# Optimization experiments

Hardware: AMD Instinct MI355X
Metric: run time of the kernel (lower is better)

Reference implementation:

```python
import jax, jax.numpy as jnp
import numpy as np

N_NODES = 20000
N_EDGES = 320000
L = 128
NODE_IN = 30
EDGE_IN = 4
NUM_LAYERS = 5


def _mlp(x, w1, b1, a, w2, b2):
    # Linear -> PReLU(scalar slope) -> Linear
    h = x @ w1 + b1
    h = jnp.where(h > 0, h, a * h)
    return h @ w2 + b2


def setup_inputs() -> dict:
    key = jax.random.key(0)
    ks = iter(jax.random.split(key, 64))
    s = 0.02

    def w(shape):
        return (s * jax.random.normal(next(ks), shape)).astype(jnp.float32)

    inp = {}
    inp["x"] = jax.random.normal(next(ks), (N_NODES, NODE_IN), dtype=jnp.float32)
    inp["edge_attr"] = jax.random.normal(next(ks), (N_EDGES, EDGE_IN), dtype=jnp.float32)
    inp["edge_index"] = jax.random.randint(next(ks), (2, N_EDGES), 0, N_NODES, dtype=jnp.int32)
    # node encoder
    inp["ne_w1"] = w((NODE_IN, L)); inp["ne_b1"] = jnp.zeros((L,), jnp.float32)
    inp["ne_a"] = jnp.float32(0.25)
    inp["ne_w2"] = w((L, L)); inp["ne_b2"] = jnp.zeros((L,), jnp.float32)
    # edge encoder
    inp["ee_w1"] = w((EDGE_IN, L)); inp["ee_b1"] = jnp.zeros((L,), jnp.float32)
    inp["ee_a"] = jnp.float32(0.25)
    inp["ee_w2"] = w((L, L)); inp["ee_b2"] = jnp.zeros((L,), jnp.float32)
    # processor layers (stacked over NUM_LAYERS)
    inp["le_w1"] = w((NUM_LAYERS, 3 * L, L)); inp["le_b1"] = jnp.zeros((NUM_LAYERS, L), jnp.float32)
    inp["le_a"] = jnp.full((NUM_LAYERS,), 0.25, jnp.float32)
    inp["le_w2"] = w((NUM_LAYERS, L, L)); inp["le_b2"] = jnp.zeros((NUM_LAYERS, L), jnp.float32)
    inp["ln_w1"] = w((NUM_LAYERS, 2 * L, L)); inp["ln_b1"] = jnp.zeros((NUM_LAYERS, L), jnp.float32)
    inp["ln_a"] = jnp.full((NUM_LAYERS,), 0.25, jnp.float32)
    inp["ln_w2"] = w((NUM_LAYERS, L, L)); inp["ln_b2"] = jnp.zeros((NUM_LAYERS, L), jnp.float32)
    # decoder
    inp["de_w1"] = w((L, L)); inp["de_b1"] = jnp.zeros((L,), jnp.float32)
    inp["de_a"] = jnp.float32(0.25)
    inp["de_w2"] = w((L, 3)); inp["de_b2"] = jnp.zeros((3,), jnp.float32)
    return inp


def reference(x, edge_attr, edge_index,
              ne_w1, ne_b1, ne_a, ne_w2, ne_b2,
              ee_w1, ee_b1, ee_a, ee_w2, ee_b2,
              le_w1, le_b1, le_a, le_w2, le_b2,
              ln_w1, ln_b1, ln_a, ln_w2, ln_b2,
              de_w1, de_b1, de_a, de_w2, de_b2):
    n = x.shape[0]
    src = edge_index[0]  # x_j (source)
    dst = edge_index[1]  # x_i (target), aggregation index

    h = _mlp(x, ne_w1, ne_b1, ne_a, ne_w2, ne_b2)            # [N, L]
    e = _mlp(edge_attr, ee_w1, ee_b1, ee_a, ee_w2, ee_b2)    # [E, L]

    for l in range(le_w1.shape[0]):
        m = jnp.concatenate([h[dst], h[src], e], axis=-1)    # [E, 3L]
        m = _mlp(m, le_w1[l], le_b1[l], le_a[l], le_w2[l], le_b2[l])  # [E, L]
        agg = jax.ops.segment_sum(m, dst, num_segments=n)    # [N, L]
        upd = _mlp(jnp.concatenate([h, agg], axis=-1),
                   ln_w1[l], ln_b1[l], ln_a[l], ln_w2[l], ln_b2[l])
        h = h + upd

    return _mlp(h, de_w1, de_b1, de_a, de_w2, de_b2)         # [N, 3]
```

## Files before the change

kernel.cpp:

```cpp
#include <hip/hip_runtime.h>
#include <cstdint>
#include <cstddef>


#define DEVI static __device__ __forceinline__

typedef __bf16 bf16_t;
typedef bf16_t bf16x8 __attribute__((ext_vector_type(8)));
typedef bf16_t bf16x4 __attribute__((ext_vector_type(4)));
typedef float f32x4v __attribute__((ext_vector_type(4)));

DEVI float4 ld4(const float* p) { return *(const float4*)p; }
DEVI void st4(float* p, float4 v) { *(float4*)p = v; }
DEVI float prelu1(float z, float a) { return z > 0.f ? z : a * z; }
DEVI void atomicAddF(float* p, float v) {
  __hip_atomic_fetch_add(p, v, __ATOMIC_RELAXED, __HIP_MEMORY_SCOPE_AGENT);
}
DEVI f32x4v mfma_bf16(bf16x8 a, bf16x8 b, f32x4v c) {
  return __builtin_amdgcn_mfma_f32_16x16x32_bf16(a, b, c, 0, 0, 0);
}
DEVI void mfma3(f32x4v& acc, bf16x8 ah, bf16x8 al, bf16x8 bh, bf16x8 bl) {
  acc = mfma_bf16(ah, bh, acc);
  acc = mfma_bf16(al, bh, acc);
  acc = mfma_bf16(ah, bl, acc);
}
DEVI void split2(float x, bf16_t& h, bf16_t& l) {
  h = (bf16_t)x;
  l = (bf16_t)(x - (float)h);
}
DEVI bf16x8 ldb8(const bf16_t* p) { return *(const bf16x8*)p; }

#define NST 136
#define EST 72


DEVI void stage_f32_c4(const float* __restrict__ src, int row0, int M,
                       int lane, int h, int cH, bf16_t* SAh, bf16_t* SAl)
{
  const int row = h * 16 + (lane >> 2);
  const int grow = row0 + row;
  const int colbase = cH * 64 + (lane & 3) * 16;
  #pragma unroll
  for (int j = 0; j < 4; ++j) {
    int kc = colbase + j * 4;
    float4 v = make_float4(0.f, 0.f, 0.f, 0.f);
    if (grow < M) v = ld4(src + (size_t)grow * 128 + kc);
    bf16_t h0,l0,h1,l1,h2,l2,h3,l3;
    split2(v.x,h0,l0); split2(v.y,h1,l1); split2(v.z,h2,l2); split2(v.w,h3,l3);
    *(bf16x4*)(SAh + row * NST + kc) = (bf16x4){h0,h1,h2,h3};
    *(bf16x4*)(SAl + row * NST + kc) = (bf16x4){l0,l1,l2,l3};
  }
}

DEVI void stage_planes_c4(const bf16_t* __restrict__ gh, const bf16_t* __restrict__ gl,
                          int row0, int M, int lane, int h, int cH,
                          bf16_t* SAh, bf16_t* SAl)
{
  const int row = h * 16 + (lane >> 2);
  const int grow = row0 + row;
  const int colbase = cH * 64 + (lane & 3) * 16;
  #pragma unroll
  for (int j = 0; j < 2; ++j) {
    int kc = colbase + j * 8;
    bf16x8 vh = {};
    bf16x8 vl = {};
    if (grow < M) {
      vh = ldb8(gh + (size_t)grow * 128 + kc);
      vl = ldb8(gl + (size_t)grow * 128 + kc);
    }
    *(bf16x8*)(SAh + row * NST + kc) = vh;
    *(bf16x8*)(SAl + row * NST + kc) = vl;
  }
}

DEVI void gemm_c4(const bf16_t* SAh, const bf16_t* SAl,
                  const bf16_t* __restrict__ BT, f32x4v acc[4],
                  int h, int ntb, int p, int q)
{
  #pragma unroll
  for (int ks = 0; ks < 4; ++ks) {
    const int k0 = ks * 32 + q * 8;
    bf16x8 aH = ldb8(SAh + (h * 16 + p) * NST + k0);
    bf16x8 aL = ldb8(SAl + (h * 16 + p) * NST + k0);
    #pragma unroll
    for (int nt = 0; nt < 4; ++nt) {
      const bf16_t* bp = BT + (size_t)((ntb + nt) * 16 + p) * 128 + k0;
      mfma3(acc[nt], aH, aL, ldb8(bp), ldb8(bp + 16384));
    }
  }
}

DEVI void store_c4(float* __restrict__ O, int row0, int M,
                   const f32x4v acc[4], int h, int cH, int p, int q)
{
  int rb = row0 + h * 16 + q * 4;
  #pragma unroll
  for (int r = 0; r < 4; ++r) {
    if (rb + r < M) {
      float* op = O + (size_t)(rb + r) * 128 + p * 8 + cH * 4;
      st4(op, make_float4(acc[0][r], acc[1][r], acc[2][r], acc[3][r]));
    }
  }
}

DEVI void stage_cregs_c4(const f32x4v acc[4], int h, int cH, int p, int q,
                         bf16_t* SAh, bf16_t* SAl)
{
  #pragma unroll
  for (int r = 0; r < 4; ++r) {
    int row = h * 16 + q * 4 + r;
    bf16x4 vh, vl;
    #pragma unroll
    for (int nt = 0; nt < 4; ++nt) {
      bf16_t hb, lb;
      split2(acc[nt][r], hb, lb);
      vh[nt] = hb; vl[nt] = lb;
    }
    *(bf16x4*)(SAh + row * NST + p * 8 + cH * 4) = vh;
    *(bf16x4*)(SAl + row * NST + p * 8 + cH * 4) = vl;
  }
}

DEVI void planes_out_c4(bf16_t* __restrict__ gh, bf16_t* __restrict__ gl,
                        int row0, int M, int lane, int h, int cH,
                        const bf16_t* SAh, const bf16_t* SAl)
{
  const int row = h * 16 + (lane >> 2);
  const int grow = row0 + row;
  const int colbase = cH * 64 + (lane & 3) * 16;
  if (grow < M) {
    #pragma unroll
    for (int j = 0; j < 2; ++j) {
      int kc = colbase + j * 8;
      *(bf16x8*)(gh + (size_t)grow * 128 + kc) = *(const bf16x8*)(SAh + row * NST + kc);
      *(bf16x8*)(gl + (size_t)grow * 128 + kc) = *(const bf16x8*)(SAl + row * NST + kc);
    }
  }
}

DEVI void ld8f(float dst[8], const float* __restrict__ src, int p) {
  *(float4*)(dst)     = ld4(src + p * 8);
  *(float4*)(dst + 4) = ld4(src + p * 8 + 4);
}

DEVI void ld4f(float dst[4], const float* __restrict__ src, int p, int cH) {
  *(float4*)(dst) = ld4(src + p * 8 + cH * 4);
}

__global__ __launch_bounds__(256, 3) void k_svu(
    float* Sbuf,
    bf16_t* __restrict__ hSh, bf16_t* __restrict__ hSl,
    const bf16_t* __restrict__ WtilT, const bf16_t* __restrict__ Wn1aT,
    const bf16_t* __restrict__ lnw2T, const bf16_t* __restrict__ W1nextT,
    const float* __restrict__ ln_b1_l, const float* __restrict__ btil_l,
    const int* __restrict__ deg, const float* __restrict__ ln_a_l,
    const float* __restrict__ ln_b2_l,
    float* __restrict__ P, float* __restrict__ Q, int doPQ, int M)
{
  __shared__ __align__(16) bf16_t SAh[32 * NST];
  __shared__ __align__(16) bf16_t SAl[32 * NST];
  const int t = threadIdx.x, lane = t & 63, wave = t >> 6;
  const int h = wave & 1, cH = wave >> 1;
  const int p = lane & 15, q = lane >> 4;
  const int row0 = blockIdx.x * 32;

  f32x4v acc1[4];
  #pragma unroll
  for (int j = 0; j < 4; ++j) acc1[j] = (f32x4v){0.f, 0.f, 0.f, 0.f};

  stage_f32_c4(Sbuf, row0, M, lane, h, cH, SAh, SAl);
  {
    const int row = h * 16 + (lane >> 2);
    const int grow = row0 + row;
    const int colbase = cH * 64 + (lane & 3) * 16;
    if (grow < M) {
      float4 z4 = make_float4(0.f, 0.f, 0.f, 0.f);
      #pragma unroll
      for (int j = 0; j < 4; ++j)
        st4(Sbuf + (size_t)grow * 128 + colbase + j * 4, z4);
    }
  }
  __syncthreads();
  gemm_c4(SAh, SAl, WtilT, acc1, h, cH * 4, p, q);
  __syncthreads();
  stage_planes_c4(hSh, hSl, row0, M, lane, h, cH, SAh, SAl);
  __syncthreads();
  gemm_c4(SAh, SAl, Wn1aT, acc1, h, cH * 4, p, q);

  float hold[4][4];
  #pragma unroll
  for (int r = 0; r < 4; ++r) {
    int row = h * 16 + q * 4 + r;
    bf16x4 vh = *(const bf16x4*)(SAh + row * NST + p * 8 + cH * 4);
    bf16x4 vl = *(const bf16x4*)(SAl + row * NST + p * 8 + cH * 4);
    #pragma unroll
    for (int nt = 0; nt < 4; ++nt)
      hold[nt][r] = (float)vh[nt] + (float)vl[nt];
  }
  __syncthreads();

  const float alpha = *ln_a_l;
  float degf[4];
  #pragma unroll
  for (int r = 0; r < 4; ++r) {
    int row = row0 + h * 16 + q * 4 + r;
    degf[r] = (row < M) ? (float)deg[row] : 0.f;
  }
  float b1c[4], btc[4];
  ld4f(b1c, ln_b1_l, p, cH);
  ld4f(btc, btil_l, p, cH);
  #pragma unroll
  for (int nt = 0; nt < 4; ++nt)
    #pragma unroll
    for (int r = 0; r < 4; ++r)
      acc1[nt][r] = prelu1(acc1[nt][r] + b1c[nt] + degf[r] * btc[nt], alpha);

  stage_cregs_c4(acc1, h, cH, p, q, SAh, SAl);
  __syncthreads();
  f32x4v acc2[4];
  #pragma unroll
  for (int j = 0; j < 4; ++j) acc2[j] = (f32x4v){0.f, 0.f, 0.f, 0.f};
  gemm_c4(SAh, SAl, lnw2T, acc2, h, cH * 4, p, q);
  __syncthreads();

  float b2c[4];
  ld4f(b2c, ln_b2_l, p, cH);
  #pragma unroll
  for (int nt = 0; nt < 4; ++nt)
    #pragma unroll
    for (int r = 0; r < 4; ++r)
      acc2[nt][r] = hold[nt][r] + acc2[nt][r] + b2c[nt];

  stage_cregs_c4(acc2, h, cH, p, q, SAh, SAl);
  __syncthreads();
  planes_out_c4(hSh, hSl, row0, M, lane, h, cH, SAh, SAl);

  if (doPQ) {
    f32x4v acc3[4];
    #pragma unroll
    for (int j = 0; j < 4; ++j) acc3[j] = (f32x4v){0.f, 0.f, 0.f, 0.f};
    gemm_c4(SAh, SAl, W1nextT, acc3, h, cH * 4, p, q);
    store_c4(P, row0, M, acc3, h, cH, p, q);
    #pragma unroll
    for (int j = 0; j < 4; ++j) acc3[j] = (f32x4v){0.f, 0.f, 0.f, 0.f};
    gemm_c4(SAh, SAl, W1nextT + 32768, acc3, h, cH * 4, p, q);
    store_c4(Q, row0, M, acc3, h, cH, p, q);
  }
}

__global__ __launch_bounds__(256, 3) void k_enc(
    const float* __restrict__ UN, const bf16_t* __restrict__ new2T,
    const float* __restrict__ b2, const bf16_t* __restrict__ W1T0,
    bf16_t* __restrict__ hSh, bf16_t* __restrict__ hSl,
    float* __restrict__ P, float* __restrict__ Q, int M)
{
  __shared__ __align__(16) bf16_t SAh[32 * NST];
  __shared__ __align__(16) bf16_t SAl[32 * NST];
  const int t = threadIdx.x, lane = t & 63, wave = t >> 6;
  const int h = wave & 1, cH = wave >> 1;
  const int p = lane & 15, q = lane >> 4;
  const int row0 = blockIdx.x * 32;

  f32x4v acc[4];
  #pragma unroll
  for (int j = 0; j < 4; ++j) acc[j] = (f32x4v){0.f, 0.f, 0.f, 0.f};
  stage_f32_c4(UN, row0, M, lane, h, cH, SAh, SAl);
  __syncthreads();
  gemm_c4(SAh, SAl, new2T, acc, h, cH * 4, p, q);
  __syncthreads();
  float b2c[4];
  ld4f(b2c, b2, p, cH);
  #pragma unroll
  for (int nt = 0; nt < 4; ++nt)
    #pragma unroll
    for (int r = 0; r < 4; ++r) acc[nt][r] += b2c[nt];
  stage_cregs_c4(acc, h, cH, p, q, SAh, SAl);
  __syncthreads();
  planes_out_c4(hSh, hSl, row0, M, lane, h, cH, SAh, SAl);

  f32x4v acc3[4];
  #pragma unroll
  for (int j = 0; j < 4; ++j) acc3[j] = (f32x4v){0.f, 0.f, 0.f, 0.f};
  gemm_c4(SAh, SAl, W1T0, acc3, h, cH * 4, p, q);
  store_c4(P, row0, M, acc3, h, cH, p, q);
  #pragma unroll
  for (int j = 0; j < 4; ++j) acc3[j] = (f32x4v){0.f, 0.f, 0.f, 0.f};
  gemm_c4(SAh, SAl, W1T0 + 32768, acc3, h, cH * 4, p, q);
  store_c4(Q, row0, M, acc3, h, cH, p, q);
}

__global__ __launch_bounds__(256, 3) void k_edge(
    const float* __restrict__ sEa, const int* __restrict__ sSrc,
    const int* __restrict__ sDst,
    const int* __restrict__ rowStart, const int* __restrict__ deg,
    const float* __restrict__ ee_w1, const float* __restrict__ ee_b1,
    const float* __restrict__ ee_a,
    const bf16_t* __restrict__ WhatT, const float* __restrict__ bvec,
    const float* __restrict__ alpha_ptr,
    const float* __restrict__ P, const float* __restrict__ Q,
    float* __restrict__ S, int N, int E)
{
  __shared__ __align__(16) float Stile[32 * 132];
  __shared__ __align__(16) float ew[640];
  __shared__ __align__(16) bf16_t Ast[128 * EST];

  const int t = threadIdx.x, lane = t & 63, wave = t >> 6;
  const int p = lane & 15, q = lane >> 4;
  const int e0 = blockIdx.x * 128;
  const int dstLo = sDst[e0];

  for (int i = t; i < 640; i += 256)
    ew[i] = (i < 512) ? ee_w1[i] : ee_b1[i - 512];
  for (int i = t; i < 32 * 132; i += 256) Stile[i] = 0.f;
  __syncthreads();

  const float ua = *ee_a;
  const float alpha = *alpha_ptr;
  float bvc[8];
  ld8f(bvc, bvec, p);

  const int srow = wave * 32 + (lane >> 1);
  const int scb = (lane & 1) * 32;
  float4 eav = make_float4(0.f, 0.f, 0.f, 0.f);
  {
    int ed = e0 + srow;
    if (ed < E) eav = ld4(sEa + (size_t)ed * 4);
  }

  f32x4v acc[2][8];
  #pragma unroll
  for (int i = 0; i < 2; ++i)
    #pragma unroll
    for (int j = 0; j < 8; ++j) acc[i][j] = (f32x4v){0.f, 0.f, 0.f, 0.f};

  for (int c = 0; c < 2; ++c) {
    #pragma unroll
    for (int j = 0; j < 8; ++j) {
      int kc = scb + j * 4;
      int kg = c * 64 + kc;
      float4 w0 = ld4(ew + kg);
      float4 w1 = ld4(ew + 128 + kg);
      float4 w2 = ld4(ew + 256 + kg);
      float4 w3 = ld4(ew + 384 + kg);
      float4 bb = ld4(ew + 512 + kg);
      float ux = bb.x, uy = bb.y, uz = bb.z, uw = bb.w;
      ux = fmaf(eav.x, w0.x, ux); uy = fmaf(eav.x, w0.y, uy);
      uz = fmaf(eav.x, w0.z, uz); uw = fmaf(eav.x, w0.w, uw);
      ux = fmaf(eav.y, w1.x, ux); uy = fmaf(eav.y, w1.y, uy);
      uz = fmaf(eav.y, w1.z, uz); uw = fmaf(eav.y, w1.w, uw);
      ux = fmaf(eav.z, w2.x, ux); uy = fmaf(eav.z, w2.y, uy);
      uz = fmaf(eav.z, w2.z, uz); uw = fmaf(eav.z, w2.w, uw);
      ux = fmaf(eav.w, w3.x, ux); uy = fmaf(eav.w, w3.y, uy);
      uz = fmaf(eav.w, w3.z, uz); uw = fmaf(eav.w, w3.w, uw);
      *(bf16x4*)(Ast + srow * EST + kc) = (bf16x4){
          (bf16_t)prelu1(ux, ua), (bf16_t)prelu1(uy, ua),
          (bf16_t)prelu1(uz, ua), (bf16_t)prelu1(uw, ua)};
    }
    #pragma unroll
    for (int ks = 0; ks < 2; ++ks) {
      const int k0 = ks * 32 + q * 8;
      const int kg = c * 64 + k0;
      bf16x8 aH0 = ldb8(Ast + (wave * 32 + p) * EST + k0);
      bf16x8 aH1 = ldb8(Ast + (wave * 32 + 16 + p) * EST + k0);
      #pragma unroll
      for (int nt = 0; nt < 8; ++nt) {
        const bf16_t* bp = WhatT + (size_t)(nt * 16 + p) * 128 + kg;
        bf16x8 bH = ldb8(bp);
        bf16x8 bL = ldb8(bp + 16384);
        acc[0][nt] = mfma_bf16(aH0, bH, acc[0][nt]);
        acc[0][nt] = mfma_bf16(aH0, bL, acc[0][nt]);
        acc[1][nt] = mfma_bf16(aH1, bH, acc[1][nt]);
        acc[1][nt] = mfma_bf16(aH1, bL, acc[1][nt]);
      }
    }
  }

  #pragma unroll
  for (int mt = 0; mt < 2; ++mt) {
    float rs[8];
    #pragma unroll
    for (int nt = 0; nt < 8; ++nt) rs[nt] = 0.f;
    int curd = -1;
    float pv[8];
    #pragma unroll
    for (int nt = 0; nt < 8; ++nt) pv[nt] = 0.f;
    #pragma unroll
    for (int r = 0; r < 4; ++r) {
      int ed = e0 + wave * 32 + mt * 16 + q * 4 + r;
      if (ed < E) {
        int d = sDst[ed];
        int s = sSrc[ed];
        if (d != curd) {
          if (curd >= 0) {
            int rr = curd - dstLo;
            if (rr < 32) {
              #pragma unroll
              for (int nt = 0; nt < 8; ++nt)
                atomicAdd(&Stile[rr * 132 + p * 8 + nt], rs[nt]);
            } else {
              #pragma unroll
              for (int nt = 0; nt < 8; ++nt)
                atomicAddF(S + (size_t)curd * 128 + p * 8 + nt, rs[nt]);
            }
            #pragma unroll
            for (int nt = 0; nt < 8; ++nt) rs[nt] = 0.f;
          }
          curd = d;
          ld8f(pv, P + (size_t)d * 128, p);
          #pragma unroll
          for (int nt = 0; nt < 8; ++nt) pv[nt] += bvc[nt];
        }
        float qv[8];
        ld8f(qv, Q + (size_t)s * 128, p);
        #pragma unroll
        for (int nt = 0; nt < 8; ++nt) {
          float z = acc[mt][nt][r] + pv[nt] + qv[nt];
          rs[nt] += prelu1(z, alpha);
        }
      }
    }
    if (curd >= 0) {
      int rr = curd - dstLo;
      if (rr < 32) {
        #pragma unroll
        for (int nt = 0; nt < 8; ++nt)
          atomicAdd(&Stile[rr * 132 + p * 8 + nt], rs[nt]);
      } else {
        #pragma unroll
        for (int nt = 0; nt < 8; ++nt)
          atomicAddF(S + (size_t)curd * 128 + p * 8 + nt, rs[nt]);
      }
    }
  }
  __syncthreads();

  const int lastE = (e0 + 127 < E) ? (e0 + 127) : (E - 1);
  const int dstHi = sDst[lastE];
  const int col4 = (t & 31) * 4;
  #pragma unroll
  for (int rr0 = 0; rr0 < 32; rr0 += 8) {
    int rr = rr0 + (t >> 5);
    int d = dstLo + rr;
    if (d <= dstHi && d < N) {
      float4 v = ld4(&Stile[rr * 132 + col4]);
      bool interior = (rowStart[d] >= e0) && (rowStart[d] + deg[d] <= e0 + 128);
      float* sp = S + (size_t)d * 128 + col4;
      if (interior) {
        st4(sp, v);
      } else {
        atomicAddF(sp + 0, v.x); atomicAddF(sp + 1, v.y);
        atomicAddF(sp + 2, v.z); atomicAddF(sp + 3, v.w);
      }
    }
  }
}

__global__ __launch_bounds__(128, 4) void k_dec(
    const bf16_t* __restrict__ hSh, const bf16_t* __restrict__ hSl,
    const bf16_t* __restrict__ dw1T,
    const float* __restrict__ de_b1, const float* __restrict__ de_a,
    const float* __restrict__ de_w2, const float* __restrict__ de_b2,
    float* __restrict__ out, int M)
{
  __shared__ __align__(16) float Cs[32][132];
  __shared__ __align__(16) float w2s[384];
  const int t = threadIdx.x, lane = t & 63, wave = t >> 6;
  const int p = lane & 15, q = lane >> 4;
  const int row0 = blockIdx.x * 32;
  for (int i = t; i < 384; i += 128) w2s[i] = de_w2[i];

  f32x4v acc[8];
  #pragma unroll
  for (int j = 0; j < 8; ++j) acc[j] = (f32x4v){0.f, 0.f, 0.f, 0.f};
  const size_t ra = (size_t)(row0 + wave * 16 + p) * 128;
  #pragma unroll
  for (int ks = 0; ks < 4; ++ks) {
    const int k0 = ks * 32 + q * 8;
    bf16x8 aH = ldb8(hSh + ra + k0);
    bf16x8 aL = ldb8(hSl + ra + k0);
    #pragma unroll
    for (int nt = 0; nt < 8; ++nt) {
      const bf16_t* bp = dw1T + (size_t)(nt * 16 + p) * 128 + k0;
      mfma3(acc[nt], aH, aL, ldb8(bp), ldb8(bp + 16384));
    }
  }
  const float alpha = *de_a;
  float b1c[8];
  ld8f(b1c, de_b1, p);
  #pragma unroll
  for (int r = 0; r < 4; ++r) {
    int row = wave * 16 + q * 4 + r;
    float* cp = &Cs[row][p * 8];
    st4(cp, make_float4(prelu1(acc[0][r] + b1c[0], alpha),
                        prelu1(acc[1][r] + b1c[1], alpha),
                        prelu1(acc[2][r] + b1c[2], alpha),
                        prelu1(acc[3][r] + b1c[3], alpha)));
    st4(cp + 4, make_float4(prelu1(acc[4][r] + b1c[4], alpha),
                            prelu1(acc[5][r] + b1c[5], alpha),
                            prelu1(acc[6][r] + b1c[6], alpha),
                            prelu1(acc[7][r] + b1c[7], alpha)));
  }
  __syncthreads();
  if (t < 32) {
    float s0 = de_b2[0], s1 = de_b2[1], s2 = de_b2[2];
    for (int k = 0; k < 128; ++k) {
      float vv = Cs[t][k];
      s0 = fmaf(vv, w2s[k * 3 + 0], s0);
      s1 = fmaf(vv, w2s[k * 3 + 1], s1);
      s2 = fmaf(vv, w2s[k * 3 + 2], s2);
    }
    int row = row0 + t;
    if (row < M) {
      out[(size_t)row * 3 + 0] = s0;
      out[(size_t)row * 3 + 1] = s1;
      out[(size_t)row * 3 + 2] = s2;
    }
  }
}

__global__ __launch_bounds__(256) void k_tsplit(
    const float* __restrict__ ne_w2, const float* __restrict__ de_w1,
    const float* __restrict__ le_w1, const float* __restrict__ ln_w1,
    const float* __restrict__ ln_w2, bf16_t* __restrict__ WT)
{
  int jid = blockIdx.x;
  const float* src; int slot;
  if (jid == 0)      { src = ne_w2; slot = 0; }
  else if (jid == 1) { src = de_w1; slot = 1; }
  else {
    int l = (jid - 2) >> 2, wj = (jid - 2) & 3;
    slot = 2 + l * 6 + wj;
    src = (wj == 0) ? le_w1 + (size_t)l * 49152
        : (wj == 1) ? le_w1 + (size_t)l * 49152 + 16384
        : (wj == 2) ? ln_w1 + (size_t)l * 32768
                    : ln_w2 + (size_t)l * 16384;
  }
  bf16_t* oh = WT + (size_t)slot * 32768;
  bf16_t* ol = oh + 16384;
  const int base = blockIdx.y * 2048;
  for (int idx = base + threadIdx.x; idx < base + 2048; idx += 256) {
    int k = idx >> 7, n = idx & 127;
    bf16_t hb, lb;
    split2(src[idx], hb, lb);
    int pos = ((n & 7) * 16 + (n >> 3)) * 128 + k;
    oh[pos] = hb;
    ol[pos] = lb;
  }
}

__global__ __launch_bounds__(256) void k_fold(
    const float* __restrict__ ee_w2, const float* __restrict__ ee_b2,
    const float* __restrict__ le_w1, const float* __restrict__ le_b1,
    const float* __restrict__ le_w2, const float* __restrict__ le_b2,
    const float* __restrict__ ln_w1,
    bf16_t* __restrict__ WT, float* __restrict__ bvec, float* __restrict__ btil)
{
  const int l = blockIdx.x;
  const int which = blockIdx.y;
  const int z = blockIdx.z;
  const float* L; const float* Rm; const float* lb; const float* badd;
  int slot; float* bout;
  if (which == 0) {
    L = ee_w2; Rm = le_w1 + (size_t)l * 49152 + 256 * 128;
    lb = ee_b2; badd = le_b1 + l * 128;
    slot = 2 + l * 6 + 4; bout = bvec + l * 128;
  } else {
    L = le_w2 + (size_t)l * 16384; Rm = ln_w1 + (size_t)l * 32768 + 128 * 128;
    lb = le_b2 + l * 128; badd = nullptr;
    slot = 2 + l * 6 + 5; bout = btil + l * 128;
  }
  bf16_t* oh = WT + (size_t)slot * 32768;
  bf16_t* ol = oh + 16384;
  const int t = threadIdx.x;
  const int base = z * 512;
  for (int eidx = base + t; eidx < base + 512; eidx += 256) {
    int k = eidx >> 7, n = eidx & 127;
    float a = 0.f;
    for (int d = 0; d < 128; d += 4) {
      float4 lv = ld4(L + k * 128 + d);
      a = fmaf(lv.x, Rm[(d + 0) * 128 + n], a);
      a = fmaf(lv.y, Rm[(d + 1) * 128 + n], a);
      a = fmaf(lv.z, Rm[(d + 2) * 128 + n], a);
      a = fmaf(lv.w, Rm[(d + 3) * 128 + n], a);
    }
    bf16_t hb, lbv;
    split2(a, hb, lbv);
    int pos = ((n & 7) * 16 + (n >> 3)) * 128 + k;
    oh[pos] = hb;
    ol[pos] = lbv;
  }
  if (z == 0 && t < 128) {
    float a = badd ? badd[t] : 0.f;
    for (int d = 0; d < 128; ++d) a = fmaf(lb[d], Rm[d * 128 + t], a);
    bout[t] = a;
  }
}

__global__ __launch_bounds__(256) void k_node_u(
    const float* __restrict__ x, const float* __restrict__ w1,
    const float* __restrict__ b1, const float* __restrict__ a_ptr,
    float* __restrict__ U, int M)
{
  int gid = blockIdx.x * 256 + threadIdx.x;
  int m = gid >> 5;
  if (m >= M) return;
  int nc = (gid & 31) << 2;
  float a = *a_ptr;
  float4 bb = ld4(b1 + nc);
  float z0 = bb.x, z1 = bb.y, z2 = bb.z, z3 = bb.w;
  const float* xr = x + (size_t)m * 30;
  #pragma unroll
  for (int j = 0; j < 30; ++j) {
    float xv = xr[j];
    float4 wv = ld4(w1 + j * 128 + nc);
    z0 = fmaf(xv, wv.x, z0); z1 = fmaf(xv, wv.y, z1);
    z2 = fmaf(xv, wv.z, z2); z3 = fmaf(xv, wv.w, z3);
  }
  st4(U + (size_t)m * 128 + nc,
      make_float4(prelu1(z0, a), prelu1(z1, a), prelu1(z2, a), prelu1(z3, a)));
}

__global__ void k_hist(const int* __restrict__ dstIdx, int* __restrict__ deg, int E) {
  int i = blockIdx.x * 256 + threadIdx.x;
  if (i < E) atomicAdd(deg + dstIdx[i], 1);
}

__global__ __launch_bounds__(1024) void k_scan(
    const int* __restrict__ deg, int* __restrict__ cursor,
    int* __restrict__ rowStart, int N, int per)
{
  __shared__ int part[1024];
  const int t = threadIdx.x;
  const int base = t * per;
  int local = 0;
  for (int i = 0; i < per; ++i) {
    int idx = base + i;
    if (idx < N) local += deg[idx];
  }
  part[t] = local;
  __syncthreads();
  for (int off = 1; off < 1024; off <<= 1) {
    int v = (t >= off) ? part[t - off] : 0;
    __syncthreads();
    part[t] += v;
    __syncthreads();
  }
  int run = (t == 0) ? 0 : part[t - 1];
  for (int i = 0; i < per; ++i) {
    int idx = base + i;
    if (idx < N) {
      cursor[idx] = run;
      rowStart[idx] = run;
      run += deg[idx];
    }
  }
}

__global__ void k_scatter(const int* __restrict__ srcIdx, const int* __restrict__ dstIdx,
                          const float* __restrict__ ea, int* __restrict__ cursor,
                          int* __restrict__ sSrc, int* __restrict__ sDst,
                          float* __restrict__ sEa, int E)
{
  int e = blockIdx.x * 256 + threadIdx.x;
  if (e < E) {
    int d = dstIdx[e];
    int p = atomicAdd(cursor + d, 1);
    sSrc[p] = srcIdx[e];
    sDst[p] = d;
    st4(sEa + (size_t)p * 4, ld4(ea + (size_t)e * 4));
  }
}

extern "C" void kernel_launch(void* const* d_in, const int* in_sizes, int n_in,
                              void* d_out, int out_size, void* d_ws, size_t ws_size,
                              hipStream_t stream)
{
  const float* x     = (const float*)d_in[0];
  const float* ea    = (const float*)d_in[1];
  const int*   ei    = (const int*)  d_in[2];
  const float* ne_w1 = (const float*)d_in[3];
  const float* ne_b1 = (const float*)d_in[4];
  const float* ne_a  = (const float*)d_in[5];
  const float* ne_w2 = (const float*)d_in[6];
  const float* ne_b2 = (const float*)d_in[7];
  const float* ee_w1 = (const float*)d_in[8];
  const float* ee_b1 = (const float*)d_in[9];
  const float* ee_a  = (const float*)d_in[10];
  const float* ee_w2 = (const float*)d_in[11];
  const float* ee_b2 = (const float*)d_in[12];
  const float* le_w1 = (const float*)d_in[13];
  const float* le_b1 = (const float*)d_in[14];
  const float* le_a  = (const float*)d_in[15];
  const float* le_w2 = (const float*)d_in[16];
  const float* le_b2 = (const float*)d_in[17];
  const float* ln_w1 = (const float*)d_in[18];
  const float* ln_b1 = (const float*)d_in[19];
  const float* ln_a  = (const float*)d_in[20];
  const float* ln_w2 = (const float*)d_in[21];
  const float* ln_b2 = (const float*)d_in[22];
  const float* de_w1 = (const float*)d_in[23];
  const float* de_b1 = (const float*)d_in[24];
  const float* de_a  = (const float*)d_in[25];
  const float* de_w2 = (const float*)d_in[26];
  const float* de_b2 = (const float*)d_in[27];

  const int N = in_sizes[0] / 30;
  const int E = in_sizes[1] / 4;
  const int* srcIdx = ei;
  const int* dstIdx = ei + E;

  const int g32 = (N + 31) / 32;
  const int gE  = (E + 127) / 128;
  const int Np = g32 * 32;
  const size_t NNp = (size_t)Np * 128;

  float* w = (float*)d_ws;
  float* Pb   = w; w += NNp;
  float* Qb   = w; w += NNp;
  float* Sb   = w; w += NNp;
  float* bvec = w; w += 5 * 128;
  float* btil = w; w += 5 * 128;
  float* sEa  = w; w += (size_t)E * 4;
  bf16_t* hSh = (bf16_t*)w;
  bf16_t* hSl = hSh + NNp;  w += NNp;
  bf16_t* WT  = (bf16_t*)w; w += 32 * 32768 / 2;
  int* ip     = (int*)w;
  int* deg    = ip; ip += N;
  int* cursor = ip; ip += N;
  int* rowStart = ip; ip += N;
  int* sSrc   = ip; ip += E;
  int* sDst   = ip; ip += E;

  float* out = (float*)d_out;

  k_tsplit<<<dim3(22, 8), dim3(256), 0, stream>>>(ne_w2, de_w1, le_w1, ln_w1, ln_w2, WT);
  k_fold<<<dim3(5, 2, 32), dim3(256), 0, stream>>>(ee_w2, ee_b2, le_w1, le_b1,
                                                   le_w2, le_b2, ln_w1, WT, bvec, btil);
  hipMemsetAsync(deg, 0, (size_t)N * 4, stream);
  k_hist<<<dim3((E + 255) / 256), dim3(256), 0, stream>>>(dstIdx, deg, E);
  k_scan<<<dim3(1), dim3(1024), 0, stream>>>(deg, cursor, rowStart, N,
                                             (N + 1023) / 1024);
  k_scatter<<<dim3((E + 255) / 256), dim3(256), 0, stream>>>(
      srcIdx, dstIdx, ea, cursor, sSrc, sDst, sEa, E);

  k_node_u<<<dim3((N * 32 + 255) / 256), dim3(256), 0, stream>>>(x, ne_w1, ne_b1, ne_a, Sb, N);
  k_enc<<<dim3(g32), dim3(256), 0, stream>>>(Sb, WT, ne_b2, WT + 2 * 32768,
                                             hSh, hSl, Pb, Qb, N);

  hipMemsetAsync(Sb, 0, (size_t)N * 128 * 4, stream);

  for (int l = 0; l < 5; ++l) {
    const bf16_t* slotL = WT + (size_t)(2 + l * 6) * 32768;
    k_edge<<<dim3(gE), dim3(256), 0, stream>>>(
        sEa, sSrc, sDst, rowStart, deg, ee_w1, ee_b1, ee_a,
        slotL + 4 * 32768, bvec + l * 128, le_a + l, Pb, Qb, Sb, N, E);
    const bf16_t* W1next = (l < 4) ? (WT + (size_t)(2 + (l + 1) * 6) * 32768) : WT;
    k_svu<<<dim3(g32), dim3(256), 0, stream>>>(
        Sb, hSh, hSl, slotL + 5 * 32768, slotL + 2 * 32768, slotL + 3 * 32768,
        W1next, ln_b1 + (size_t)l * 128, btil + l * 128, deg, ln_a + l,
        ln_b2 + (size_t)l * 128, Pb, Qb, (l < 4) ? 1 : 0, N);
  }

  k_dec<<<dim3(g32), dim3(128), 0, stream>>>(hSh, hSl, WT + 32768, de_b1, de_a,
                                             de_w2, de_b2, out, N);
}
```

Before: 1.334 ms.

## Fuse node encoder first layer into k_enc and decoder into last k_svu

Computes the node encoder's first linear+PReLU inside k_enc from shared-memory copies of x and ne_w1, so the separate k_node_u kernel and its fp32 intermediate round trip go away. The final update layer now also runs the decoder MLP in place, skipping the hSh/hSl write and the separate k_dec launch. k_edge's launch-bounds occupancy hint is raised from 3 to 4 blocks. The extra shared memory in k_enc and the larger k_svu could lower occupancy, and the raised k_edge hint may cause register spilling.

```diff
diff --git a/kernel.cpp b/kernel.cpp
--- a/kernel.cpp
+++ b/kernel.cpp
@@ -155,10 +155,18 @@
     const float* __restrict__ ln_b1_l, const float* __restrict__ btil_l,
     const int* __restrict__ deg, const float* __restrict__ ln_a_l,
     const float* __restrict__ ln_b2_l,
-    float* __restrict__ P, float* __restrict__ Q, int doPQ, int M)
-{
-  __shared__ __align__(16) bf16_t SAh[32 * NST];
-  __shared__ __align__(16) bf16_t SAl[32 * NST];
+    float* __restrict__ P, float* __restrict__ Q, int doPQ,
+    const bf16_t* __restrict__ dw1T, const float* __restrict__ de_b1,
+    const float* __restrict__ de_a, const float* __restrict__ de_w2,
+    const float* __restrict__ de_b2, float* __restrict__ outp,
+    int doDec, int M)
+{
+  __shared__ __align__(16) char SMEM[2 * 32 * NST * 2];
+  __shared__ __align__(16) float w2s[384];
+  bf16_t* SAh = (bf16_t*)SMEM;
+  bf16_t* SAl = (bf16_t*)(SMEM + 32 * NST * 2);
+  float*  Cs  = (float*)SMEM;
+
   const int t = threadIdx.x, lane = t & 63, wave = t >> 6;
   const int h = wave & 1, cH = wave >> 1;
   const int p = lane & 15, q = lane >> 4;
@@ -232,6 +240,50 @@
       acc2[nt][r] = hold[nt][r] + acc2[nt][r] + b2c[nt];
 
   stage_cregs_c4(acc2, h, cH, p, q, SAh, SAl);
+
+  if (doDec) {
+    if (t < 128) {
+      w2s[t] = de_w2[t]; w2s[t + 128] = de_w2[t + 128]; w2s[t + 256] = de_w2[t + 256];
+    }
+    __syncthreads();
+    f32x4v acc3[4];
+    #pragma unroll
+    for (int j = 0; j < 4; ++j) acc3[j] = (f32x4v){0.f, 0.f, 0.f, 0.f};
+    gemm_c4(SAh, SAl, dw1T, acc3, h, cH * 4, p, q);
+    const float da = *de_a;
+    float db1[4];
+    ld4f(db1, de_b1, p, cH);
+    #pragma unroll
+    for (int nt = 0; nt < 4; ++nt)
+      #pragma unroll
+      for (int r = 0; r < 4; ++r)
+        acc3[nt][r] = prelu1(acc3[nt][r] + db1[nt], da);
+    __syncthreads();
+    #pragma unroll
+    for (int r = 0; r < 4; ++r) {
+      int row = h * 16 + q * 4 + r;
+      st4(&Cs[row * 132 + p * 8 + cH * 4],
+          make_float4(acc3[0][r], acc3[1][r], acc3[2][r], acc3[3][r]));
+    }
+    __syncthreads();
+    if (t < 32) {
+      float s0 = de_b2[0], s1 = de_b2[1], s2 = de_b2[2];
+      for (int k = 0; k < 128; ++k) {
+        float vv = Cs[t * 132 + k];
+        s0 = fmaf(vv, w2s[k * 3 + 0], s0);
+        s1 = fmaf(vv, w2s[k * 3 + 1], s1);
+        s2 = fmaf(vv, w2s[k * 3 + 2], s2);
+      }
+      int row = row0 + t;
+      if (row < M) {
+        outp[(size_t)row * 3 + 0] = s0;
+        outp[(size_t)row * 3 + 1] = s1;
+        outp[(size_t)row * 3 + 2] = s2;
+      }
+    }
+    return;
+  }
+
   __syncthreads();
   planes_out_c4(hSh, hSl, row0, M, lane, h, cH, SAh, SAl);
 
@@ -249,23 +301,65 @@
 }
 
 __global__ __launch_bounds__(256, 3) void k_enc(
-    const float* __restrict__ UN, const bf16_t* __restrict__ new2T,
+    const float* __restrict__ x, const float* __restrict__ ne_w1,
+    const float* __restrict__ ne_b1, const float* __restrict__ ne_a,
+    const bf16_t* __restrict__ new2T,
     const float* __restrict__ b2, const bf16_t* __restrict__ W1T0,
     bf16_t* __restrict__ hSh, bf16_t* __restrict__ hSl,
     float* __restrict__ P, float* __restrict__ Q, int M)
 {
   __shared__ __align__(16) bf16_t SAh[32 * NST];
   __shared__ __align__(16) bf16_t SAl[32 * NST];
+  __shared__ __align__(16) float w1s[30 * 128];
+  __shared__ __align__(16) float xs[32 * 30];
+  __shared__ __align__(16) float b1s[128];
   const int t = threadIdx.x, lane = t & 63, wave = t >> 6;
   const int h = wave & 1, cH = wave >> 1;
   const int p = lane & 15, q = lane >> 4;
   const int row0 = blockIdx.x * 32;
 
+  for (int i = t; i < 30 * 128; i += 256) w1s[i] = ne_w1[i];
+  {
+    int nrow = M - row0; if (nrow > 32) nrow = 32;
+    int cnt = nrow * 30;
+    for (int i = t; i < cnt; i += 256) xs[i] = x[(size_t)row0 * 30 + i];
+  }
+  if (t < 128) b1s[t] = ne_b1[t];
+  __syncthreads();
+  const float ua = *ne_a;
+
+  {
+    const int row = h * 16 + (lane >> 2);
+    const int grow = row0 + row;
+    const int colbase = cH * 64 + (lane & 3) * 16;
+    #pragma unroll
+    for (int jj = 0; jj < 4; ++jj) {
+      int kc = colbase + jj * 4;
+      float z0 = 0.f, z1 = 0.f, z2 = 0.f, z3 = 0.f;
+      if (grow < M) {
+        float4 bb = ld4(b1s + kc);
+        z0 = bb.x; z1 = bb.y; z2 = bb.z; z3 = bb.w;
+        #pragma unroll
+        for (int j = 0; j < 30; ++j) {
+          float xv = xs[row * 30 + j];
+          float4 wv = ld4(w1s + j * 128 + kc);
+          z0 = fmaf(xv, wv.x, z0); z1 = fmaf(xv, wv.y, z1);
+          z2 = fmaf(xv, wv.z, z2); z3 = fmaf(xv, wv.w, z3);
+        }
+        z0 = prelu1(z0, ua); z1 = prelu1(z1, ua);
+        z2 = prelu1(z2, ua); z3 = prelu1(z3, ua);
+      }
+      bf16_t h0,l0,h1,l1,h2,l2,h3,l3;
+      split2(z0,h0,l0); split2(z1,h1,l1); split2(z2,h2,l2); split2(z3,h3,l3);
+      *(bf16x4*)(SAh + row * NST + kc) = (bf16x4){h0,h1,h2,h3};
+      *(bf16x4*)(SAl + row * NST + kc) = (bf16x4){l0,l1,l2,l3};
+    }
+  }
+  __syncthreads();
+
   f32x4v acc[4];
   #pragma unroll
   for (int j = 0; j < 4; ++j) acc[j] = (f32x4v){0.f, 0.f, 0.f, 0.f};
-  stage_f32_c4(UN, row0, M, lane, h, cH, SAh, SAl);
-  __syncthreads();
   gemm_c4(SAh, SAl, new2T, acc, h, cH * 4, p, q);
   __syncthreads();
   float b2c[4];
@@ -289,7 +383,7 @@
   store_c4(Q, row0, M, acc3, h, cH, p, q);
 }
 
-__global__ __launch_bounds__(256, 3) void k_edge(
+__global__ __launch_bounds__(256, 4) void k_edge(
     const float* __restrict__ sEa, const int* __restrict__ sSrc,
     const int* __restrict__ sDst,
     const int* __restrict__ rowStart, const int* __restrict__ deg,
@@ -455,69 +549,6 @@
   }
 }
 
-__global__ __launch_bounds__(128, 4) void k_dec(
-    const bf16_t* __restrict__ hSh, const bf16_t* __restrict__ hSl,
-    const bf16_t* __restrict__ dw1T,
-    const float* __restrict__ de_b1, const float* __restrict__ de_a,
-    const float* __restrict__ de_w2, const float* __restrict__ de_b2,
-    float* __restrict__ out, int M)
-{
-  __shared__ __align__(16) float Cs[32][132];
-  __shared__ __align__(16) float w2s[384];
-  const int t = threadIdx.x, lane = t & 63, wave = t >> 6;
-  const int p = lane & 15, q = lane >> 4;
-  const int row0 = blockIdx.x * 32;
-  for (int i = t; i < 384; i += 128) w2s[i] = de_w2[i];
-
-  f32x4v acc[8];
-  #pragma unroll
-  for (int j = 0; j < 8; ++j) acc[j] = (f32x4v){0.f, 0.f, 0.f, 0.f};
-  const size_t ra = (size_t)(row0 + wave * 16 + p) * 128;
-  #pragma unroll
-  for (int ks = 0; ks < 4; ++ks) {
-    const int k0 = ks * 32 + q * 8;
-    bf16x8 aH = ldb8(hSh + ra + k0);
-    bf16x8 aL = ldb8(hSl + ra + k0);
-    #pragma unroll
-    for (int nt = 0; nt < 8; ++nt) {
-      const bf16_t* bp = dw1T + (size_t)(nt * 16 + p) * 128 + k0;
-      mfma3(acc[nt], aH, aL, ldb8(bp), ldb8(bp + 16384));
-    }
-  }
-  const float alpha = *de_a;
-  float b1c[8];
-  ld8f(b1c, de_b1, p);
-  #pragma unroll
-  for (int r = 0; r < 4; ++r) {
-    int row = wave * 16 + q * 4 + r;
-    float* cp = &Cs[row][p * 8];
-    st4(cp, make_float4(prelu1(acc[0][r] + b1c[0], alpha),
-                        prelu1(acc[1][r] + b1c[1], alpha),
-                        prelu1(acc[2][r] + b1c[2], alpha),
-                        prelu1(acc[3][r] + b1c[3], alpha)));
-    st4(cp + 4, make_float4(prelu1(acc[4][r] + b1c[4], alpha),
-                            prelu1(acc[5][r] + b1c[5], alpha),
-                            prelu1(acc[6][r] + b1c[6], alpha),
-                            prelu1(acc[7][r] + b1c[7], alpha)));
-  }
-  __syncthreads();
-  if (t < 32) {
-    float s0 = de_b2[0], s1 = de_b2[1], s2 = de_b2[2];
-    for (int k = 0; k < 128; ++k) {
-      float vv = Cs[t][k];
-      s0 = fmaf(vv, w2s[k * 3 + 0], s0);
-      s1 = fmaf(vv, w2s[k * 3 + 1], s1);
-      s2 = fmaf(vv, w2s[k * 3 + 2], s2);
-    }
-    int row = row0 + t;
-    if (row < M) {
-      out[(size_t)row * 3 + 0] = s0;
-      out[(size_t)row * 3 + 1] = s1;
-      out[(size_t)row * 3 + 2] = s2;
-    }
-  }
-}
-
 __global__ __launch_bounds__(256) void k_tsplit(
     const float* __restrict__ ne_w2, const float* __restrict__ de_w1,
     const float* __restrict__ le_w1, const float* __restrict__ ln_w1,
@@ -594,30 +625,6 @@
     for (int d = 0; d < 128; ++d) a = fmaf(lb[d], Rm[d * 128 + t], a);
     bout[t] = a;
   }
-}
-
-__global__ __launch_bounds__(256) void k_node_u(
-    const float* __restrict__ x, const float* __restrict__ w1,
-    const float* __restrict__ b1, const float* __restrict__ a_ptr,
-    float* __restrict__ U, int M)
-{
-  int gid = blockIdx.x * 256 + threadIdx.x;
-  int m = gid >> 5;
-  if (m >= M) return;
-  int nc = (gid & 31) << 2;
-  float a = *a_ptr;
-  float4 bb = ld4(b1 + nc);
-  float z0 = bb.x, z1 = bb.y, z2 = bb.z, z3 = bb.w;
-  const float* xr = x + (size_t)m * 30;
-  #pragma unroll
-  for (int j = 0; j < 30; ++j) {
-    float xv = xr[j];
-    float4 wv = ld4(w1 + j * 128 + nc);
-    z0 = fmaf(xv, wv.x, z0); z1 = fmaf(xv, wv.y, z1);
-    z2 = fmaf(xv, wv.z, z2); z3 = fmaf(xv, wv.w, z3);
-  }
-  st4(U + (size_t)m * 128 + nc,
-      make_float4(prelu1(z0, a), prelu1(z1, a), prelu1(z2, a), prelu1(z3, a)));
 }
 
 __global__ void k_hist(const int* __restrict__ dstIdx, int* __restrict__ deg, int E) {
@@ -743,8 +750,8 @@
   k_scatter<<<dim3((E + 255) / 256), dim3(256), 0, stream>>>(
       srcIdx, dstIdx, ea, cursor, sSrc, sDst, sEa, E);
 
-  k_node_u<<<dim3((N * 32 + 255) / 256), dim3(256), 0, stream>>>(x, ne_w1, ne_b1, ne_a, Sb, N);
-  k_enc<<<dim3(g32), dim3(256), 0, stream>>>(Sb, WT, ne_b2, WT + 2 * 32768,
+  k_enc<<<dim3(g32), dim3(256), 0, stream>>>(x, ne_w1, ne_b1, ne_a,
+                                             WT, ne_b2, WT + 2 * 32768,
                                              hSh, hSl, Pb, Qb, N);
 
   hipMemsetAsync(Sb, 0, (size_t)N * 128 * 4, stream);
@@ -758,9 +765,8 @@
     k_svu<<<dim3(g32), dim3(256), 0, stream>>>(
         Sb, hSh, hSl, slotL + 5 * 32768, slotL + 2 * 32768, slotL + 3 * 32768,
         W1next, ln_b1 + (size_t)l * 128, btil + l * 128, deg, ln_a + l,
-        ln_b2 + (size_t)l * 128, Pb, Qb, (l < 4) ? 1 : 0, N);
-  }
-
-  k_dec<<<dim3(g32), dim3(128), 0, stream>>>(hSh, hSl, WT + 32768, de_b1, de_a,
-                                             de_w2, de_b2, out, N);
-}
+        ln_b2 + (size_t)l * 128, Pb, Qb, (l < 4) ? 1 : 0,
+        WT + 32768, de_b1, de_a, de_w2, de_b2, out,
+        (l == 4) ? 1 : 0, N);
+  }
+}
```

Measured after the change: 1.328 ms. No clear change (-0.5%).
